# Optimization experiments

Hardware: AMD Instinct MI355X
Metric: run time of the kernel (lower is better)

The kernel has to match this reference:

```python
import jax, jax.numpy as jnp
import numpy as np

NUM_HEADS = 16
D_MODEL = 1024
HEAD_DIM = D_MODEL // NUM_HEADS
B, S = 2, 2048


def setup_inputs() -> dict:
    key = jax.random.key(0)
    ks = jax.random.split(key, 11)
    scale = 1.0 / np.sqrt(D_MODEL)
    inp = {
        'query': jax.random.normal(ks[0], (B, S, D_MODEL), jnp.float32),
        'key': jax.random.normal(ks[1], (B, S, D_MODEL), jnp.float32),
        'value': jax.random.normal(ks[2], (B, S, D_MODEL), jnp.float32),
        'Wq': jax.random.normal(ks[3], (D_MODEL, D_MODEL), jnp.float32) * scale,
        'bq': jnp.zeros((D_MODEL,), jnp.float32),
        'Wk': jax.random.normal(ks[4], (D_MODEL, D_MODEL), jnp.float32) * scale,
        'bk': jnp.zeros((D_MODEL,), jnp.float32),
        'Wv': jax.random.normal(ks[5], (D_MODEL, D_MODEL), jnp.float32) * scale,
        'bv': jnp.zeros((D_MODEL,), jnp.float32),
        'Wo': jax.random.normal(ks[6], (D_MODEL, D_MODEL), jnp.float32) * scale,
        'bo': jnp.zeros((D_MODEL,), jnp.float32),
    }
    return inp


def reference(query, key, value, Wq, bq, Wk, bk, Wv, bv, Wo, bo):
    b, s, _ = query.shape
    # Linear projections (torch Linear: x @ W.T + b; here W stored as [in,out])
    Q = query @ Wq + bq
    K = key @ Wk + bk
    V = value @ Wv + bv
    # [B, H, S, Dh]
    Q = Q.reshape(b, s, NUM_HEADS, HEAD_DIM).transpose(0, 2, 1, 3)
    K = K.reshape(b, -1, NUM_HEADS, HEAD_DIM).transpose(0, 2, 1, 3)
    V = V.reshape(b, -1, NUM_HEADS, HEAD_DIM).transpose(0, 2, 1, 3)
    scores = jnp.einsum('bhqd,bhkd->bhqk', Q, K) / jnp.sqrt(jnp.float32(HEAD_DIM)).astype(Q.dtype)
    attn = jax.nn.softmax(scores, axis=-1)
    ctx = jnp.einsum('bhqk,bhkd->bhqd', attn, V)
    ctx = ctx.transpose(0, 2, 1, 3).reshape(b, s, D_MODEL)
    return ctx @ Wo + bo
```

## Files before the change

### kernel.cpp

```cpp
#include <hip/hip_runtime.h>
#include <hip/hip_bf16.h>
#include <math.h>

#define NUM_HEADS 16
#define D_MODEL 1024
#define HEAD_DIM 64
#define BATCH 2
#define SEQ 2048
#define M_TOTAL (BATCH*SEQ)

typedef __bf16 bf16;
typedef __bf16 bf16x2 __attribute__((ext_vector_type(2)));
typedef __bf16 bf16x4 __attribute__((ext_vector_type(4)));
typedef __bf16 bf16x8 __attribute__((ext_vector_type(8)));
typedef float  floatx4  __attribute__((ext_vector_type(4)));
typedef float  floatx16 __attribute__((ext_vector_type(16)));
typedef unsigned int uintx2 __attribute__((ext_vector_type(2)));
typedef unsigned int uintx4 __attribute__((ext_vector_type(4)));

#define CLSCALE 0.180336884f

#if __has_builtin(__builtin_amdgcn_exp2f)
#define EXP2(x) __builtin_amdgcn_exp2f(x)
#else
#define EXP2(x) exp2f(x)
#endif

__device__ __forceinline__ void async_copy16(const bf16* g, bf16* l) {
    __builtin_amdgcn_global_load_lds(
        (const __attribute__((address_space(1))) void*)g,
        (__attribute__((address_space(3))) void*)l, 16, 0, 0);
}

__device__ __forceinline__ unsigned pk2(float lo, float hi) {
    bf16x2 t; t[0] = (bf16)lo; t[1] = (bf16)hi;
    return __builtin_bit_cast(unsigned, t);
}

__global__ __launch_bounds__(256)
void convert_kernel(const float* __restrict__ Wq, const float* __restrict__ Wk,
                    const float* __restrict__ Wv, const float* __restrict__ Wo,
                    const float* __restrict__ q, const float* __restrict__ k,
                    const float* __restrict__ v,
                    bf16* __restrict__ Wt, bf16* __restrict__ Xb)
{
    const int blk = blockIdx.x;
    const int tid = threadIdx.x;
    if (blk < 256) {
        const int wi  = blk >> 6;
        const int sub = blk & 63;
        const int xb  = sub & 3;
        const int yb  = sub >> 2;
        const float* W = (wi == 0) ? Wq : (wi == 1) ? Wk : (wi == 2) ? Wv : Wo;
        bf16* dstM = Wt + (size_t)wi * D_MODEL * D_MODEL;
        const int n  = xb * 256 + tid;
        const int k0 = yb * 64;
        bf16* dst = dstM + (size_t)n * D_MODEL + k0;
        #pragma unroll
        for (int jc = 0; jc < 8; ++jc) {
            bf16x8 w;
            #pragma unroll
            for (int j = 0; j < 8; ++j)
                w[j] = (bf16)W[(size_t)(k0 + jc * 8 + j) * D_MODEL + n];
            *(bf16x8*)(dst + jc * 8) = w;
        }
    } else {
        const int rem   = blk - 256;
        const int plane = rem >> 11;
        const int xb    = rem & 2047;
        const float* X = (plane == 0) ? q : (plane == 1) ? k : v;
        bf16* dst = Xb + (size_t)plane * M_TOTAL * D_MODEL;
        size_t i = ((size_t)xb * 256 + tid) * 8;
        const float4 u = *(const float4*)(X + i);
        const float4 w = *(const float4*)(X + i + 4);
        bf16x8 o;
        o[0] = (bf16)u.x; o[1] = (bf16)u.y; o[2] = (bf16)u.z; o[3] = (bf16)u.w;
        o[4] = (bf16)w.x; o[5] = (bf16)w.y; o[6] = (bf16)w.z; o[7] = (bf16)w.w;
        *(bf16x8*)(dst + i) = o;
    }
}

__global__ __launch_bounds__(256)
void proj_kernel(const bf16* __restrict__ Xb, const bf16* __restrict__ Wt,
                 const float* __restrict__ bq, const float* __restrict__ bk,
                 const float* __restrict__ bv,
                 bf16* __restrict__ Qo, bf16* __restrict__ Ko, bf16* __restrict__ Vto)
{
    const int lin  = blockIdx.x;
    const int xcd  = lin & 7;
    const int idx  = lin >> 3;
    const int nt   = idx & 7;
    const int t2   = idx >> 3;
    const int mloc = t2 & 3;
    const int which= t2 >> 2;
    const int tileM = (xcd * 4 + mloc) * 128;
    const int tileN = nt * 128;

    const bf16* X     = Xb + (size_t)which * M_TOTAL * D_MODEL;
    const bf16* Wm    = Wt + (size_t)which * D_MODEL * D_MODEL;
    const float* bias = (which == 0) ? bq : (which == 1) ? bk : bv;

    const int tid  = threadIdx.x;
    const int lane = tid & 63;
    const int wave = tid >> 6;
    const int quad = lane >> 4;
    const int l16  = lane & 15;

    __shared__ bf16 sA[2][4096];
    __shared__ bf16 sB[2][4096];

    floatx4 acc[4][4];
    const floatx4 z4 = {0.0f, 0.0f, 0.0f, 0.0f};
    #pragma unroll
    for (int i = 0; i < 4; i++)
        #pragma unroll
        for (int j = 0; j < 4; j++) acc[i][j] = z4;

    const int rC = ((tid >> 6) & 3) * 16 + (tid & 15);
    const int cC = ((tid >> 4) & 3) * 8;
    const bf16* gA0 = X  + (size_t)(tileM + rC) * D_MODEL + cC;
    const bf16* gA1 = gA0 + (size_t)64 * D_MODEL;
    const bf16* gB0 = Wm + (size_t)(tileN + rC) * D_MODEL + cC;
    const bf16* gB1 = gB0 + (size_t)64 * D_MODEL;

    async_copy16(gA0, &sA[0][tid * 8]);
    async_copy16(gA1, &sA[0][(tid + 256) * 8]);
    async_copy16(gB0, &sB[0][tid * 8]);
    async_copy16(gB1, &sB[0][(tid + 256) * 8]);

    const int fA = (wave >> 1) * 4;
    const int fB = (wave & 1) * 4;

    for (int kt = 0; kt < 32; ++kt) {
        const int p = kt & 1;
        __syncthreads();

        bf16x8 af[4], bfr[4];
        #pragma unroll
        for (int i = 0; i < 4; i++) af[i]  = *(const bf16x8*)&sA[p][((fA + i) * 64 + lane) * 8];
        #pragma unroll
        for (int j = 0; j < 4; j++) bfr[j] = *(const bf16x8*)&sB[p][((fB + j) * 64 + lane) * 8];

        if (kt < 31) {
            const int k0 = (kt + 1) * 32;
            async_copy16(gA0 + k0, &sA[p ^ 1][tid * 8]);
            async_copy16(gA1 + k0, &sA[p ^ 1][(tid + 256) * 8]);
            async_copy16(gB0 + k0, &sB[p ^ 1][tid * 8]);
            async_copy16(gB1 + k0, &sB[p ^ 1][(tid + 256) * 8]);
        }

        if (which != 2) {
            #pragma unroll
            for (int i = 0; i < 4; i++)
                #pragma unroll
                for (int j = 0; j < 4; j++)
                    acc[i][j] = __builtin_amdgcn_mfma_f32_16x16x32_bf16(af[i], bfr[j], acc[i][j], 0, 0, 0);
        } else {
            #pragma unroll
            for (int i = 0; i < 4; i++)
                #pragma unroll
                for (int j = 0; j < 4; j++)
                    acc[i][j] = __builtin_amdgcn_mfma_f32_16x16x32_bf16(bfr[i], af[j], acc[i][j], 0, 0, 0);
        }
    }

    const int wm = (wave >> 1) * 64;
    const int wn = (wave & 1) * 64;

    if (which != 2) {
        bf16* out = (which == 0) ? Qo : Ko;
        const float oscale = (which == 0) ? CLSCALE : 1.0f;
        #pragma unroll
        for (int i = 0; i < 4; i++) {
            int mbase = tileM + wm + i * 16 + quad * 4;
            #pragma unroll
            for (int j = 0; j < 4; j++) {
                int n = tileN + wn + j * 16 + l16;
                float bb = bias[n];
                int h = n >> 6, d = n & 63;
                #pragma unroll
                for (int r = 0; r < 4; r++) {
                    int mm = mbase + r;
                    int b = mm >> 11, s = mm & 2047;
                    out[(((size_t)(b * NUM_HEADS + h)) * SEQ + s) * HEAD_DIM + d] =
                        (bf16)((acc[i][j][r] + bb) * oscale);
                }
            }
        }
    } else {
        #pragma unroll
        for (int i = 0; i < 4; i++) {
            #pragma unroll
            for (int r = 0; r < 4; r++) {
                int n = tileN + wn + i * 16 + quad * 4 + r;
                float bb = bias[n];
                int h = n >> 6, d = n & 63;
                #pragma unroll
                for (int j = 0; j < 4; j++) {
                    int m = tileM + wm + j * 16 + l16;
                    int b = m >> 11, s = m & 2047;
                    Vto[(((size_t)(b * NUM_HEADS + h)) * HEAD_DIM + d) * SEQ + s] =
                        (bf16)(acc[i][j][r] + bb);
                }
            }
        }
    }
}

__global__ __launch_bounds__(256)
void attn_kernel(const bf16* __restrict__ Q, const bf16* __restrict__ K,
                 const bf16* __restrict__ Vt, bf16* __restrict__ Ctx)
{
    const int lin    = blockIdx.x;
    const int xcd    = lin & 7;
    const int rest   = lin >> 3;
    const int superg = rest >> 5;
    const int qi     = rest & 31;
    const int bh     = superg * 8 + xcd;
    const int b      = bh >> 4, h = bh & 15;
    const int q0     = qi * 64;

    const int tid  = threadIdx.x;
    const int lane = tid & 63;
    const int wave = tid >> 6;
    const int half = lane >> 5;
    const int m31  = lane & 31;
    const int xs   = m31 & 7;

    const int qsub  = wave & 1;
    const int kjsub = wave >> 1;

    __shared__ bf16 sK[2][64 * 64];
    __shared__ bf16 sV[2][64 * 64];
    __shared__ float sL[64];

    const bf16* Qb  = Q  + ((size_t)bh * SEQ + q0) * HEAD_DIM;
    const bf16* Kb  = K  + (size_t)bh * SEQ * HEAD_DIM;
    const bf16* Vtb = Vt + (size_t)bh * HEAD_DIM * SEQ;

    bf16x8 bQ[4];
    #pragma unroll
    for (int s = 0; s < 4; s++)
        bQ[s] = *(const bf16x8*)(Qb + (size_t)(qsub * 32 + m31) * HEAD_DIM + s * 16 + half * 8);

    #pragma unroll
    for (int it = 0; it < 2; ++it) {
        int c    = tid + it * 256;
        int row  = c >> 3;
        int scol = ((c & 7) ^ (row & 7)) * 8;
        async_copy16(Kb  + (size_t)row * HEAD_DIM + scol, &sK[0][c * 8]);
        async_copy16(Vtb + (size_t)row * SEQ + scol,      &sV[0][c * 8]);
    }

    floatx16 o0, o1;
    #pragma unroll
    for (int r = 0; r < 16; r++) { o0[r] = 0.0f; o1[r] = 0.0f; }
    float lp = 0.0f;

    for (int kt = 0; kt < SEQ / 64; ++kt) {
        const int p = kt & 1;
        __syncthreads();

        bf16x8 aK[4];
        #pragma unroll
        for (int s = 0; s < 4; s++)
            aK[s] = *(const bf16x8*)&sK[p][(kjsub * 32 + m31) * 64 + (((2 * s + half) ^ xs) * 8)];

        if (kt + 1 < SEQ / 64) {
            #pragma unroll
            for (int it = 0; it < 2; ++it) {
                int c    = tid + it * 256;
                int row  = c >> 3;
                int scol = ((c & 7) ^ (row & 7)) * 8;
                async_copy16(Kb  + (size_t)((kt + 1) * 64 + row) * HEAD_DIM + scol,
                             &sK[p ^ 1][c * 8]);
                async_copy16(Vtb + (size_t)row * SEQ + (kt + 1) * 64 + scol,
                             &sV[p ^ 1][c * 8]);
            }
        }

        floatx16 sc;
        #pragma unroll
        for (int r = 0; r < 16; r++) sc[r] = 0.0f;
        __builtin_amdgcn_s_setprio(1);
        #pragma unroll
        for (int s = 0; s < 4; s++)
            sc = __builtin_amdgcn_mfma_f32_32x32x16_bf16(aK[s], bQ[s], sc, 0, 0, 0);
        __builtin_amdgcn_s_setprio(0);

        #pragma unroll
        for (int r = 0; r < 16; r++) sc[r] = EXP2(sc[r]);
        float ls = 0.0f;
        #pragma unroll
        for (int r = 0; r < 16; r++) ls += sc[r];
        lp += ls;

        bf16x8 bP[2];
        #pragma unroll
        for (int s = 0; s < 2; s++) {
            const int bs = 8 * s;
            unsigned x = pk2(sc[bs + 0], sc[bs + 1]);
            unsigned z = pk2(sc[bs + 2], sc[bs + 3]);
            unsigned y = pk2(sc[bs + 4], sc[bs + 5]);
            unsigned w = pk2(sc[bs + 6], sc[bs + 7]);
            auto r0 = __builtin_amdgcn_permlane32_swap(x, y, false, false);
            auto r1 = __builtin_amdgcn_permlane32_swap(z, w, false, false);
            uintx4 bp;
            bp[0] = r0[0]; bp[1] = r1[0]; bp[2] = r0[1]; bp[3] = r1[1];
            bP[s] = __builtin_bit_cast(bf16x8, bp);
        }

        __builtin_amdgcn_s_setprio(1);
        #pragma unroll
        for (int s = 0; s < 2; s++) {
            int ch = ((4 * kjsub + 2 * s + half) ^ xs) * 8;
            bf16x8 a0 = *(const bf16x8*)&sV[p][(size_t)m31 * 64 + ch];
            bf16x8 a1 = *(const bf16x8*)&sV[p][(size_t)(32 + m31) * 64 + ch];
            o0 = __builtin_amdgcn_mfma_f32_32x32x16_bf16(a0, bP[s], o0, 0, 0, 0);
            o1 = __builtin_amdgcn_mfma_f32_32x32x16_bf16(a1, bP[s], o1, 0, 0, 0);
        }
        __builtin_amdgcn_s_setprio(0);
    }

    lp += __shfl_xor(lp, 32, 64);

    __syncthreads();
    float* fO = (qsub == 0) ? (float*)&sK[0][0] : (float*)&sK[1][0];
    if (kjsub == 1) {
        #pragma unroll
        for (int r = 0; r < 16; r++) {
            fO[r * 64 + lane]        = o0[r];
            fO[1024 + r * 64 + lane] = o1[r];
        }
        if (half == 0) sL[qsub * 32 + m31] = lp;
    }
    __syncthreads();
    if (kjsub == 0) {
        #pragma unroll
        for (int r = 0; r < 16; r++) {
            o0[r] += fO[r * 64 + lane];
            o1[r] += fO[1024 + r * 64 + lane];
        }
        float denom = lp + sL[qsub * 32 + m31];
        float inv = 1.0f / denom;

        int q = q0 + qsub * 32 + m31;
        size_t base = ((size_t)b * SEQ + q) * D_MODEL + h * HEAD_DIM;
        #pragma unroll
        for (int rg = 0; rg < 4; rg++) {
            int d0 = rg * 8 + half * 4;
            bf16x4 w0, w1;
            #pragma unroll
            for (int i = 0; i < 4; i++) {
                w0[i] = (bf16)(o0[rg * 4 + i] * inv);
                w1[i] = (bf16)(o1[rg * 4 + i] * inv);
            }
            *(bf16x4*)&Ctx[base + d0]      = w0;
            *(bf16x4*)&Ctx[base + 32 + d0] = w1;
        }
    }
}

__global__ __launch_bounds__(256)
void out_proj_kernel(const bf16* __restrict__ A, const bf16* __restrict__ Wto,
                     const float* __restrict__ bias, float* __restrict__ Out)
{
    const int lin  = blockIdx.x;
    const int xcd  = lin & 7;
    const int idx  = lin >> 3;
    const int nt   = idx & 7;
    const int mloc = idx >> 3;
    const int tileM = (xcd * 8 + mloc) * 64;
    const int tileN = nt * 128;

    const int tid  = threadIdx.x;
    const int lane = tid & 63;
    const int wave = tid >> 6;
    const int quad = lane >> 4;
    const int l16  = lane & 15;

    __shared__ bf16 sA[2][2048];
    __shared__ bf16 sB[2][4096];

    floatx4 acc[2][4];
    const floatx4 z4 = {0.0f, 0.0f, 0.0f, 0.0f};
    #pragma unroll
    for (int i = 0; i < 2; i++)
        #pragma unroll
        for (int j = 0; j < 4; j++) acc[i][j] = z4;

    const int rA = ((tid >> 7) & 1) * 32 + ((tid >> 6) & 1) * 16 + (tid & 15);
    const int rB = ((tid >> 6) & 3) * 16 + (tid & 15);
    const int cC = ((tid >> 4) & 3) * 8;
    const bf16* gA0 = A   + (size_t)(tileM + rA) * D_MODEL + cC;
    const bf16* gB0 = Wto + (size_t)(tileN + rB) * D_MODEL + cC;
    const bf16* gB1 = gB0 + (size_t)64 * D_MODEL;

    async_copy16(gA0, &sA[0][tid * 8]);
    async_copy16(gB0, &sB[0][tid * 8]);
    async_copy16(gB1, &sB[0][(tid + 256) * 8]);

    const int fA = (wave >> 1) * 2;
    const int fB = (wave & 1) * 4;

    for (int kt = 0; kt < 32; ++kt) {
        const int p = kt & 1;
        __syncthreads();

        bf16x8 af[2], bfr[4];
        #pragma unroll
        for (int i = 0; i < 2; i++) af[i]  = *(const bf16x8*)&sA[p][((fA + i) * 64 + lane) * 8];
        #pragma unroll
        for (int j = 0; j < 4; j++) bfr[j] = *(const bf16x8*)&sB[p][((fB + j) * 64 + lane) * 8];

        if (kt < 31) {
            const int k0 = (kt + 1) * 32;
            async_copy16(gA0 + k0, &sA[p ^ 1][tid * 8]);
            async_copy16(gB0 + k0, &sB[p ^ 1][tid * 8]);
            async_copy16(gB1 + k0, &sB[p ^ 1][(tid + 256) * 8]);
        }

        #pragma unroll
        for (int i = 0; i < 2; i++)
            #pragma unroll
            for (int j = 0; j < 4; j++)
                acc[i][j] = __builtin_amdgcn_mfma_f32_16x16x32_bf16(af[i], bfr[j], acc[i][j], 0, 0, 0);
    }

    const int wm = (wave >> 1) * 32;
    const int wn = (wave & 1) * 64;

    #pragma unroll
    for (int i = 0; i < 2; i++) {
        int mbase = tileM + wm + i * 16 + quad * 4;
        #pragma unroll
        for (int j = 0; j < 4; j++) {
            int n = tileN + wn + j * 16 + l16;
            float bb = bias[n];
            #pragma unroll
            for (int r = 0; r < 4; r++)
                Out[(size_t)(mbase + r) * D_MODEL + n] = acc[i][j][r] + bb;
        }
    }
}

extern "C" void kernel_launch(void* const* d_in, const int* in_sizes, int n_in,
                              void* d_out, int out_size, void* d_ws, size_t ws_size,
                              hipStream_t stream)
{
    const float* q  = (const float*)d_in[0];
    const float* k  = (const float*)d_in[1];
    const float* v  = (const float*)d_in[2];
    const float* Wq = (const float*)d_in[3];
    const float* bq = (const float*)d_in[4];
    const float* Wk = (const float*)d_in[5];
    const float* bk = (const float*)d_in[6];
    const float* Wv = (const float*)d_in[7];
    const float* bv = (const float*)d_in[8];
    const float* Wo = (const float*)d_in[9];
    const float* bo = (const float*)d_in[10];
    float* out = (float*)d_out;

    const size_t PLANE = (size_t)M_TOTAL * D_MODEL;
    bf16* Qb = (bf16*)d_ws;
    bf16* Kb = Qb + PLANE;
    bf16* Vt = Kb + PLANE;
    bf16* Cb = Vt + PLANE;
    bf16* Wt = Cb + PLANE;
    bf16* Xb = Wt + 4 * (size_t)D_MODEL * D_MODEL;

    convert_kernel<<<dim3(6400), 256, 0, stream>>>(Wq, Wk, Wv, Wo, q, k, v, Wt, Xb);
    proj_kernel<<<dim3(768), 256, 0, stream>>>(Xb, Wt, bq, bk, bv, Qb, Kb, Vt);
    attn_kernel<<<dim3(1024), 256, 0, stream>>>(Qb, Kb, Vt, Cb);
    out_proj_kernel<<<dim3(512), 256, 0, stream>>>(Cb, Wt + 3 * (size_t)D_MODEL * D_MODEL, bo, out);
}
```

Measured before the change: 254.4 us.

## Triple-buffer QKV and output projection GEMM loads with partial vmcnt waits

Both projection GEMM kernels now use three shared-memory stages and prefetch two k-tiles ahead. The full __syncthreads is replaced by an explicit s_waitcnt vmcnt(N) plus s_barrier, so only the oldest stage has to land before compute. The aim is to hide global-to-LDS copy latency behind the MFMA work. In exchange it uses 1.5x the LDS, which may lower occupancy, and it relies on the vmcnt counts matching the number of async copies issued per stage.

```diff
diff --git a/kernel.cpp b/kernel.cpp
--- a/kernel.cpp
+++ b/kernel.cpp
@@ -106,8 +106,8 @@
     const int quad = lane >> 4;
     const int l16  = lane & 15;
 
-    __shared__ bf16 sA[2][4096];
-    __shared__ bf16 sB[2][4096];
+    __shared__ bf16 sA[3][4096];
+    __shared__ bf16 sB[3][4096];
 
     floatx4 acc[4][4];
     const floatx4 z4 = {0.0f, 0.0f, 0.0f, 0.0f};
@@ -123,17 +123,25 @@
     const bf16* gB0 = Wm + (size_t)(tileN + rC) * D_MODEL + cC;
     const bf16* gB1 = gB0 + (size_t)64 * D_MODEL;
 
-    async_copy16(gA0, &sA[0][tid * 8]);
-    async_copy16(gA1, &sA[0][(tid + 256) * 8]);
-    async_copy16(gB0, &sB[0][tid * 8]);
-    async_copy16(gB1, &sB[0][(tid + 256) * 8]);
+    auto stage = [&](int buf, int k0) {
+        async_copy16(gA0 + k0, &sA[buf][tid * 8]);
+        async_copy16(gA1 + k0, &sA[buf][(tid + 256) * 8]);
+        async_copy16(gB0 + k0, &sB[buf][tid * 8]);
+        async_copy16(gB1 + k0, &sB[buf][(tid + 256) * 8]);
+    };
+
+    stage(0, 0);
+    stage(1, 32);
 
     const int fA = (wave >> 1) * 4;
     const int fB = (wave & 1) * 4;
 
+    int p = 0;
     for (int kt = 0; kt < 32; ++kt) {
-        const int p = kt & 1;
-        __syncthreads();
+        if (kt < 31) asm volatile("s_waitcnt vmcnt(4)" ::: "memory");
+        else         asm volatile("s_waitcnt vmcnt(0)" ::: "memory");
+        __builtin_amdgcn_s_barrier();
+        __builtin_amdgcn_sched_barrier(0);
 
         bf16x8 af[4], bfr[4];
         #pragma unroll
@@ -141,12 +149,9 @@
         #pragma unroll
         for (int j = 0; j < 4; j++) bfr[j] = *(const bf16x8*)&sB[p][((fB + j) * 64 + lane) * 8];
 
-        if (kt < 31) {
-            const int k0 = (kt + 1) * 32;
-            async_copy16(gA0 + k0, &sA[p ^ 1][tid * 8]);
-            async_copy16(gA1 + k0, &sA[p ^ 1][(tid + 256) * 8]);
-            async_copy16(gB0 + k0, &sB[p ^ 1][tid * 8]);
-            async_copy16(gB1 + k0, &sB[p ^ 1][(tid + 256) * 8]);
+        if (kt + 2 < 32) {
+            int pw = p + 2; if (pw >= 3) pw -= 3;
+            stage(pw, (kt + 2) * 32);
         }
 
         if (which != 2) {
@@ -162,6 +167,7 @@
                 for (int j = 0; j < 4; j++)
                     acc[i][j] = __builtin_amdgcn_mfma_f32_16x16x32_bf16(bfr[i], af[j], acc[i][j], 0, 0, 0);
         }
+        p = (p == 2) ? 0 : p + 1;
     }
 
     const int wm = (wave >> 1) * 64;
@@ -379,8 +385,8 @@
     const int quad = lane >> 4;
     const int l16  = lane & 15;
 
-    __shared__ bf16 sA[2][2048];
-    __shared__ bf16 sB[2][4096];
+    __shared__ bf16 sA[3][2048];
+    __shared__ bf16 sB[3][4096];
 
     floatx4 acc[2][4];
     const floatx4 z4 = {0.0f, 0.0f, 0.0f, 0.0f};
@@ -396,16 +402,24 @@
     const bf16* gB0 = Wto + (size_t)(tileN + rB) * D_MODEL + cC;
     const bf16* gB1 = gB0 + (size_t)64 * D_MODEL;
 
-    async_copy16(gA0, &sA[0][tid * 8]);
-    async_copy16(gB0, &sB[0][tid * 8]);
-    async_copy16(gB1, &sB[0][(tid + 256) * 8]);
+    auto stage = [&](int buf, int k0) {
+        async_copy16(gA0 + k0, &sA[buf][tid * 8]);
+        async_copy16(gB0 + k0, &sB[buf][tid * 8]);
+        async_copy16(gB1 + k0, &sB[buf][(tid + 256) * 8]);
+    };
+
+    stage(0, 0);
+    stage(1, 32);
 
     const int fA = (wave >> 1) * 2;
     const int fB = (wave & 1) * 4;
 
+    int p = 0;
     for (int kt = 0; kt < 32; ++kt) {
-        const int p = kt & 1;
-        __syncthreads();
+        if (kt < 31) asm volatile("s_waitcnt vmcnt(3)" ::: "memory");
+        else         asm volatile("s_waitcnt vmcnt(0)" ::: "memory");
+        __builtin_amdgcn_s_barrier();
+        __builtin_amdgcn_sched_barrier(0);
 
         bf16x8 af[2], bfr[4];
         #pragma unroll
@@ -413,11 +427,9 @@
         #pragma unroll
         for (int j = 0; j < 4; j++) bfr[j] = *(const bf16x8*)&sB[p][((fB + j) * 64 + lane) * 8];
 
-        if (kt < 31) {
-            const int k0 = (kt + 1) * 32;
-            async_copy16(gA0 + k0, &sA[p ^ 1][tid * 8]);
-            async_copy16(gB0 + k0, &sB[p ^ 1][tid * 8]);
-            async_copy16(gB1 + k0, &sB[p ^ 1][(tid + 256) * 8]);
+        if (kt + 2 < 32) {
+            int pw = p + 2; if (pw >= 3) pw -= 3;
+            stage(pw, (kt + 2) * 32);
         }
 
         #pragma unroll
@@ -425,6 +437,7 @@
             #pragma unroll
             for (int j = 0; j < 4; j++)
                 acc[i][j] = __builtin_amdgcn_mfma_f32_16x16x32_bf16(af[i], bfr[j], acc[i][j], 0, 0, 0);
+        p = (p == 2) ? 0 : p + 1;
     }
 
     const int wm = (wave >> 1) * 32;
```

New measurement: 252.3 us. Within noise of the previous version (-0.8%).

## Fuse fp32-to-bf16 activation conversion into projection GEMM and single-buffer GEMM tiles

Applied to the files above, without the earlier changes.

The separate pass that converts the query, key and value activations to bf16 is removed. The projection GEMM now loads fp32 activations directly, converts them in registers and stores bf16 into shared memory, which avoids writing and re-reading a full bf16 copy of the inputs. Both the projection and output-projection GEMMs also drop double-buffered shared-memory prefetch in favour of a single buffer with two barriers per k-step. That frees LDS but exposes global-load latency that the prefetch used to hide.

```diff
diff --git a/kernel.cpp b/kernel.cpp
--- a/kernel.cpp
+++ b/kernel.cpp
@@ -15,7 +15,6 @@
 typedef __bf16 bf16x8 __attribute__((ext_vector_type(8)));
 typedef float  floatx4  __attribute__((ext_vector_type(4)));
 typedef float  floatx16 __attribute__((ext_vector_type(16)));
-typedef unsigned int uintx2 __attribute__((ext_vector_type(2)));
 typedef unsigned int uintx4 __attribute__((ext_vector_type(4)));
 
 #define CLSCALE 0.180336884f
@@ -40,48 +39,32 @@
 __global__ __launch_bounds__(256)
 void convert_kernel(const float* __restrict__ Wq, const float* __restrict__ Wk,
                     const float* __restrict__ Wv, const float* __restrict__ Wo,
-                    const float* __restrict__ q, const float* __restrict__ k,
-                    const float* __restrict__ v,
-                    bf16* __restrict__ Wt, bf16* __restrict__ Xb)
+                    bf16* __restrict__ Wt)
 {
     const int blk = blockIdx.x;
     const int tid = threadIdx.x;
-    if (blk < 256) {
-        const int wi  = blk >> 6;
-        const int sub = blk & 63;
-        const int xb  = sub & 3;
-        const int yb  = sub >> 2;
-        const float* W = (wi == 0) ? Wq : (wi == 1) ? Wk : (wi == 2) ? Wv : Wo;
-        bf16* dstM = Wt + (size_t)wi * D_MODEL * D_MODEL;
-        const int n  = xb * 256 + tid;
-        const int k0 = yb * 64;
-        bf16* dst = dstM + (size_t)n * D_MODEL + k0;
-        #pragma unroll
-        for (int jc = 0; jc < 8; ++jc) {
-            bf16x8 w;
-            #pragma unroll
-            for (int j = 0; j < 8; ++j)
-                w[j] = (bf16)W[(size_t)(k0 + jc * 8 + j) * D_MODEL + n];
-            *(bf16x8*)(dst + jc * 8) = w;
-        }
-    } else {
-        const int rem   = blk - 256;
-        const int plane = rem >> 11;
-        const int xb    = rem & 2047;
-        const float* X = (plane == 0) ? q : (plane == 1) ? k : v;
-        bf16* dst = Xb + (size_t)plane * M_TOTAL * D_MODEL;
-        size_t i = ((size_t)xb * 256 + tid) * 8;
-        const float4 u = *(const float4*)(X + i);
-        const float4 w = *(const float4*)(X + i + 4);
-        bf16x8 o;
-        o[0] = (bf16)u.x; o[1] = (bf16)u.y; o[2] = (bf16)u.z; o[3] = (bf16)u.w;
-        o[4] = (bf16)w.x; o[5] = (bf16)w.y; o[6] = (bf16)w.z; o[7] = (bf16)w.w;
-        *(bf16x8*)(dst + i) = o;
+    const int wi  = blk >> 6;
+    const int sub = blk & 63;
+    const int xb  = sub & 3;
+    const int yb  = sub >> 2;
+    const float* W = (wi == 0) ? Wq : (wi == 1) ? Wk : (wi == 2) ? Wv : Wo;
+    bf16* dstM = Wt + (size_t)wi * D_MODEL * D_MODEL;
+    const int n  = xb * 256 + tid;
+    const int k0 = yb * 64;
+    bf16* dst = dstM + (size_t)n * D_MODEL + k0;
+    #pragma unroll
+    for (int jc = 0; jc < 8; ++jc) {
+        bf16x8 w;
+        #pragma unroll
+        for (int j = 0; j < 8; ++j)
+            w[j] = (bf16)W[(size_t)(k0 + jc * 8 + j) * D_MODEL + n];
+        *(bf16x8*)(dst + jc * 8) = w;
     }
 }
 
 __global__ __launch_bounds__(256)
-void proj_kernel(const bf16* __restrict__ Xb, const bf16* __restrict__ Wt,
+void proj_kernel(const float* __restrict__ Xq, const float* __restrict__ Xk,
+                 const float* __restrict__ Xv, const bf16* __restrict__ Wt,
                  const float* __restrict__ bq, const float* __restrict__ bk,
                  const float* __restrict__ bv,
                  bf16* __restrict__ Qo, bf16* __restrict__ Ko, bf16* __restrict__ Vto)
@@ -96,7 +79,7 @@
     const int tileM = (xcd * 4 + mloc) * 128;
     const int tileN = nt * 128;
 
-    const bf16* X     = Xb + (size_t)which * M_TOTAL * D_MODEL;
+    const float* X32  = (which == 0) ? Xq : (which == 1) ? Xk : Xv;
     const bf16* Wm    = Wt + (size_t)which * D_MODEL * D_MODEL;
     const float* bias = (which == 0) ? bq : (which == 1) ? bk : bv;
 
@@ -106,8 +89,8 @@
     const int quad = lane >> 4;
     const int l16  = lane & 15;
 
-    __shared__ bf16 sA[2][4096];
-    __shared__ bf16 sB[2][4096];
+    __shared__ bf16 sA[4096];
+    __shared__ bf16 sB[4096];
 
     floatx4 acc[4][4];
     const floatx4 z4 = {0.0f, 0.0f, 0.0f, 0.0f};
@@ -118,36 +101,40 @@
 
     const int rC = ((tid >> 6) & 3) * 16 + (tid & 15);
     const int cC = ((tid >> 4) & 3) * 8;
-    const bf16* gA0 = X  + (size_t)(tileM + rC) * D_MODEL + cC;
-    const bf16* gA1 = gA0 + (size_t)64 * D_MODEL;
-    const bf16* gB0 = Wm + (size_t)(tileN + rC) * D_MODEL + cC;
-    const bf16* gB1 = gB0 + (size_t)64 * D_MODEL;
-
-    async_copy16(gA0, &sA[0][tid * 8]);
-    async_copy16(gA1, &sA[0][(tid + 256) * 8]);
-    async_copy16(gB0, &sB[0][tid * 8]);
-    async_copy16(gB1, &sB[0][(tid + 256) * 8]);
+    const float* gA0 = X32 + (size_t)(tileM + rC) * D_MODEL + cC;
+    const float* gA1 = gA0 + (size_t)64 * D_MODEL;
+    const bf16*  gB0 = Wm  + (size_t)(tileN + rC) * D_MODEL + cC;
+    const bf16*  gB1 = gB0 + (size_t)64 * D_MODEL;
 
     const int fA = (wave >> 1) * 4;
     const int fB = (wave & 1) * 4;
 
     for (int kt = 0; kt < 32; ++kt) {
-        const int p = kt & 1;
+        const int k0 = kt * 32;
         __syncthreads();
 
+        async_copy16(gB0 + k0, &sB[tid * 8]);
+        async_copy16(gB1 + k0, &sB[(tid + 256) * 8]);
+
+        float4 u0 = *(const float4*)(gA0 + k0);
+        float4 v0 = *(const float4*)(gA0 + k0 + 4);
+        float4 u1 = *(const float4*)(gA1 + k0);
+        float4 v1 = *(const float4*)(gA1 + k0 + 4);
+        bf16x8 a0, a1;
+        a0[0] = (bf16)u0.x; a0[1] = (bf16)u0.y; a0[2] = (bf16)u0.z; a0[3] = (bf16)u0.w;
+        a0[4] = (bf16)v0.x; a0[5] = (bf16)v0.y; a0[6] = (bf16)v0.z; a0[7] = (bf16)v0.w;
+        a1[0] = (bf16)u1.x; a1[1] = (bf16)u1.y; a1[2] = (bf16)u1.z; a1[3] = (bf16)u1.w;
+        a1[4] = (bf16)v1.x; a1[5] = (bf16)v1.y; a1[6] = (bf16)v1.z; a1[7] = (bf16)v1.w;
+        *(bf16x8*)&sA[tid * 8]         = a0;
+        *(bf16x8*)&sA[(tid + 256) * 8] = a1;
+
+        __syncthreads();
+
         bf16x8 af[4], bfr[4];
         #pragma unroll
-        for (int i = 0; i < 4; i++) af[i]  = *(const bf16x8*)&sA[p][((fA + i) * 64 + lane) * 8];
-        #pragma unroll
-        for (int j = 0; j < 4; j++) bfr[j] = *(const bf16x8*)&sB[p][((fB + j) * 64 + lane) * 8];
-
-        if (kt < 31) {
-            const int k0 = (kt + 1) * 32;
-            async_copy16(gA0 + k0, &sA[p ^ 1][tid * 8]);
-            async_copy16(gA1 + k0, &sA[p ^ 1][(tid + 256) * 8]);
-            async_copy16(gB0 + k0, &sB[p ^ 1][tid * 8]);
-            async_copy16(gB1 + k0, &sB[p ^ 1][(tid + 256) * 8]);
-        }
+        for (int i = 0; i < 4; i++) af[i]  = *(const bf16x8*)&sA[((fA + i) * 64 + lane) * 8];
+        #pragma unroll
+        for (int j = 0; j < 4; j++) bfr[j] = *(const bf16x8*)&sB[((fB + j) * 64 + lane) * 8];
 
         if (which != 2) {
             #pragma unroll
@@ -379,8 +366,8 @@
     const int quad = lane >> 4;
     const int l16  = lane & 15;
 
-    __shared__ bf16 sA[2][2048];
-    __shared__ bf16 sB[2][4096];
+    __shared__ bf16 sA[2048];
+    __shared__ bf16 sB[4096];
 
     floatx4 acc[2][4];
     const floatx4 z4 = {0.0f, 0.0f, 0.0f, 0.0f};
@@ -389,36 +376,30 @@
         #pragma unroll
         for (int j = 0; j < 4; j++) acc[i][j] = z4;
 
-    const int rA = ((tid >> 7) & 1) * 32 + ((tid >> 6) & 1) * 16 + (tid & 15);
-    const int rB = ((tid >> 6) & 3) * 16 + (tid & 15);
+    const int rC = ((tid >> 6) & 3) * 16 + (tid & 15);
     const int cC = ((tid >> 4) & 3) * 8;
-    const bf16* gA0 = A   + (size_t)(tileM + rA) * D_MODEL + cC;
-    const bf16* gB0 = Wto + (size_t)(tileN + rB) * D_MODEL + cC;
+    const bf16* gA0 = A   + (size_t)(tileM + rC) * D_MODEL + cC;
+    const bf16* gB0 = Wto + (size_t)(tileN + rC) * D_MODEL + cC;
     const bf16* gB1 = gB0 + (size_t)64 * D_MODEL;
-
-    async_copy16(gA0, &sA[0][tid * 8]);
-    async_copy16(gB0, &sB[0][tid * 8]);
-    async_copy16(gB1, &sB[0][(tid + 256) * 8]);
 
     const int fA = (wave >> 1) * 2;
     const int fB = (wave & 1) * 4;
 
     for (int kt = 0; kt < 32; ++kt) {
-        const int p = kt & 1;
+        const int k0 = kt * 32;
         __syncthreads();
 
+        async_copy16(gA0 + k0, &sA[tid * 8]);
+        async_copy16(gB0 + k0, &sB[tid * 8]);
+        async_copy16(gB1 + k0, &sB[(tid + 256) * 8]);
+
+        __syncthreads();
+
         bf16x8 af[2], bfr[4];
         #pragma unroll
-        for (int i = 0; i < 2; i++) af[i]  = *(const bf16x8*)&sA[p][((fA + i) * 64 + lane) * 8];
-        #pragma unroll
-        for (int j = 0; j < 4; j++) bfr[j] = *(const bf16x8*)&sB[p][((fB + j) * 64 + lane) * 8];
-
-        if (kt < 31) {
-            const int k0 = (kt + 1) * 32;
-            async_copy16(gA0 + k0, &sA[p ^ 1][tid * 8]);
-            async_copy16(gB0 + k0, &sB[p ^ 1][tid * 8]);
-            async_copy16(gB1 + k0, &sB[p ^ 1][(tid + 256) * 8]);
-        }
+        for (int i = 0; i < 2; i++) af[i]  = *(const bf16x8*)&sA[((fA + i) * 64 + lane) * 8];
+        #pragma unroll
+        for (int j = 0; j < 4; j++) bfr[j] = *(const bf16x8*)&sB[((fB + j) * 64 + lane) * 8];
 
         #pragma unroll
         for (int i = 0; i < 2; i++)
@@ -467,10 +448,9 @@
     bf16* Vt = Kb + PLANE;
     bf16* Cb = Vt + PLANE;
     bf16* Wt = Cb + PLANE;
-    bf16* Xb = Wt + 4 * (size_t)D_MODEL * D_MODEL;
-
-    convert_kernel<<<dim3(6400), 256, 0, stream>>>(Wq, Wk, Wv, Wo, q, k, v, Wt, Xb);
-    proj_kernel<<<dim3(768), 256, 0, stream>>>(Xb, Wt, bq, bk, bv, Qb, Kb, Vt);
+
+    convert_kernel<<<dim3(256), 256, 0, stream>>>(Wq, Wk, Wv, Wo, Wt);
+    proj_kernel<<<dim3(768), 256, 0, stream>>>(q, k, v, Wt, bq, bk, bv, Qb, Kb, Vt);
     attn_kernel<<<dim3(1024), 256, 0, stream>>>(Qb, Kb, Vt, Cb);
     out_proj_kernel<<<dim3(512), 256, 0, stream>>>(Cb, Wt + 3 * (size_t)D_MODEL * D_MODEL, bo, out);
 }
```

Result: slower. 291.8 us (+14.7%).

## Shrink projection GEMM tiles and drop double buffering for more blocks

Applied to the files above, without the earlier changes.

The QKV projection tile goes from 128x128 to 64x128 and the output projection tile from 64x128 to 64x64, doubling the grid sizes of both kernels. The LDS double buffer with prefetch is replaced by a single buffer, loaded and then synchronised before compute on every k step. The intent is more blocks and occupancy with less LDS per block. In exchange, global loads no longer overlap with MFMA work, there are two barriers per iteration, and operand reuse per block is lower.

```diff
diff --git a/kernel.cpp b/kernel.cpp
--- a/kernel.cpp
+++ b/kernel.cpp
@@ -15,7 +15,6 @@
 typedef __bf16 bf16x8 __attribute__((ext_vector_type(8)));
 typedef float  floatx4  __attribute__((ext_vector_type(4)));
 typedef float  floatx16 __attribute__((ext_vector_type(16)));
-typedef unsigned int uintx2 __attribute__((ext_vector_type(2)));
 typedef unsigned int uintx4 __attribute__((ext_vector_type(4)));
 
 #define CLSCALE 0.180336884f
@@ -91,9 +90,9 @@
     const int idx  = lin >> 3;
     const int nt   = idx & 7;
     const int t2   = idx >> 3;
-    const int mloc = t2 & 3;
-    const int which= t2 >> 2;
-    const int tileM = (xcd * 4 + mloc) * 128;
+    const int mloc = t2 & 7;
+    const int which= t2 >> 3;
+    const int tileM = (xcd * 8 + mloc) * 64;
     const int tileN = nt * 128;
 
     const bf16* X     = Xb + (size_t)which * M_TOTAL * D_MODEL;
@@ -106,72 +105,64 @@
     const int quad = lane >> 4;
     const int l16  = lane & 15;
 
-    __shared__ bf16 sA[2][4096];
-    __shared__ bf16 sB[2][4096];
-
-    floatx4 acc[4][4];
+    __shared__ bf16 sA[4 * 64 * 8];
+    __shared__ bf16 sB[8 * 64 * 8];
+
+    floatx4 acc[2][4];
     const floatx4 z4 = {0.0f, 0.0f, 0.0f, 0.0f};
     #pragma unroll
-    for (int i = 0; i < 4; i++)
+    for (int i = 0; i < 2; i++)
         #pragma unroll
         for (int j = 0; j < 4; j++) acc[i][j] = z4;
 
     const int rC = ((tid >> 6) & 3) * 16 + (tid & 15);
     const int cC = ((tid >> 4) & 3) * 8;
-    const bf16* gA0 = X  + (size_t)(tileM + rC) * D_MODEL + cC;
-    const bf16* gA1 = gA0 + (size_t)64 * D_MODEL;
+    const bf16* gA  = X  + (size_t)(tileM + rC) * D_MODEL + cC;
     const bf16* gB0 = Wm + (size_t)(tileN + rC) * D_MODEL + cC;
     const bf16* gB1 = gB0 + (size_t)64 * D_MODEL;
 
-    async_copy16(gA0, &sA[0][tid * 8]);
-    async_copy16(gA1, &sA[0][(tid + 256) * 8]);
-    async_copy16(gB0, &sB[0][tid * 8]);
-    async_copy16(gB1, &sB[0][(tid + 256) * 8]);
-
-    const int fA = (wave >> 1) * 4;
+    const int fA = (wave >> 1) * 2;
     const int fB = (wave & 1) * 4;
 
     for (int kt = 0; kt < 32; ++kt) {
-        const int p = kt & 1;
+        const int k0 = kt * 32;
         __syncthreads();
 
-        bf16x8 af[4], bfr[4];
-        #pragma unroll
-        for (int i = 0; i < 4; i++) af[i]  = *(const bf16x8*)&sA[p][((fA + i) * 64 + lane) * 8];
-        #pragma unroll
-        for (int j = 0; j < 4; j++) bfr[j] = *(const bf16x8*)&sB[p][((fB + j) * 64 + lane) * 8];
-
-        if (kt < 31) {
-            const int k0 = (kt + 1) * 32;
-            async_copy16(gA0 + k0, &sA[p ^ 1][tid * 8]);
-            async_copy16(gA1 + k0, &sA[p ^ 1][(tid + 256) * 8]);
-            async_copy16(gB0 + k0, &sB[p ^ 1][tid * 8]);
-            async_copy16(gB1 + k0, &sB[p ^ 1][(tid + 256) * 8]);
-        }
+        async_copy16(gA  + k0, &sA[tid * 8]);
+        async_copy16(gB0 + k0, &sB[tid * 8]);
+        async_copy16(gB1 + k0, &sB[(tid + 256) * 8]);
+
+        __syncthreads();
+
+        bf16x8 af[2], bfr[4];
+        #pragma unroll
+        for (int i = 0; i < 2; i++) af[i]  = *(const bf16x8*)&sA[((fA + i) * 64 + lane) * 8];
+        #pragma unroll
+        for (int j = 0; j < 4; j++) bfr[j] = *(const bf16x8*)&sB[((fB + j) * 64 + lane) * 8];
 
         if (which != 2) {
             #pragma unroll
-            for (int i = 0; i < 4; i++)
+            for (int i = 0; i < 2; i++)
                 #pragma unroll
                 for (int j = 0; j < 4; j++)
                     acc[i][j] = __builtin_amdgcn_mfma_f32_16x16x32_bf16(af[i], bfr[j], acc[i][j], 0, 0, 0);
         } else {
             #pragma unroll
-            for (int i = 0; i < 4; i++)
+            for (int i = 0; i < 2; i++)
                 #pragma unroll
                 for (int j = 0; j < 4; j++)
-                    acc[i][j] = __builtin_amdgcn_mfma_f32_16x16x32_bf16(bfr[i], af[j], acc[i][j], 0, 0, 0);
-        }
-    }
-
-    const int wm = (wave >> 1) * 64;
+                    acc[i][j] = __builtin_amdgcn_mfma_f32_16x16x32_bf16(bfr[j], af[i], acc[i][j], 0, 0, 0);
+        }
+    }
+
+    const int wm = (wave >> 1) * 32;
     const int wn = (wave & 1) * 64;
 
     if (which != 2) {
         bf16* out = (which == 0) ? Qo : Ko;
         const float oscale = (which == 0) ? CLSCALE : 1.0f;
         #pragma unroll
-        for (int i = 0; i < 4; i++) {
+        for (int i = 0; i < 2; i++) {
             int mbase = tileM + wm + i * 16 + quad * 4;
             #pragma unroll
             for (int j = 0; j < 4; j++) {
@@ -189,15 +180,15 @@
         }
     } else {
         #pragma unroll
-        for (int i = 0; i < 4; i++) {
+        for (int j = 0; j < 4; j++) {
             #pragma unroll
             for (int r = 0; r < 4; r++) {
-                int n = tileN + wn + i * 16 + quad * 4 + r;
+                int n = tileN + wn + j * 16 + quad * 4 + r;
                 float bb = bias[n];
                 int h = n >> 6, d = n & 63;
                 #pragma unroll
-                for (int j = 0; j < 4; j++) {
-                    int m = tileM + wm + j * 16 + l16;
+                for (int i = 0; i < 2; i++) {
+                    int m = tileM + wm + i * 16 + l16;
                     int b = m >> 11, s = m & 2047;
                     Vto[(((size_t)(b * NUM_HEADS + h)) * HEAD_DIM + d) * SEQ + s] =
                         (bf16)(acc[i][j][r] + bb);
@@ -368,10 +359,10 @@
     const int lin  = blockIdx.x;
     const int xcd  = lin & 7;
     const int idx  = lin >> 3;
-    const int nt   = idx & 7;
-    const int mloc = idx >> 3;
+    const int nt   = idx & 15;
+    const int mloc = idx >> 4;
     const int tileM = (xcd * 8 + mloc) * 64;
-    const int tileN = nt * 128;
+    const int tileN = nt * 64;
 
     const int tid  = threadIdx.x;
     const int lane = tid & 63;
@@ -379,62 +370,54 @@
     const int quad = lane >> 4;
     const int l16  = lane & 15;
 
-    __shared__ bf16 sA[2][2048];
-    __shared__ bf16 sB[2][4096];
-
-    floatx4 acc[2][4];
+    __shared__ bf16 sA[4 * 64 * 8];
+    __shared__ bf16 sB[4 * 64 * 8];
+
+    floatx4 acc[2][2];
     const floatx4 z4 = {0.0f, 0.0f, 0.0f, 0.0f};
     #pragma unroll
     for (int i = 0; i < 2; i++)
         #pragma unroll
-        for (int j = 0; j < 4; j++) acc[i][j] = z4;
-
-    const int rA = ((tid >> 7) & 1) * 32 + ((tid >> 6) & 1) * 16 + (tid & 15);
-    const int rB = ((tid >> 6) & 3) * 16 + (tid & 15);
+        for (int j = 0; j < 2; j++) acc[i][j] = z4;
+
+    const int rC = ((tid >> 6) & 3) * 16 + (tid & 15);
     const int cC = ((tid >> 4) & 3) * 8;
-    const bf16* gA0 = A   + (size_t)(tileM + rA) * D_MODEL + cC;
-    const bf16* gB0 = Wto + (size_t)(tileN + rB) * D_MODEL + cC;
-    const bf16* gB1 = gB0 + (size_t)64 * D_MODEL;
-
-    async_copy16(gA0, &sA[0][tid * 8]);
-    async_copy16(gB0, &sB[0][tid * 8]);
-    async_copy16(gB1, &sB[0][(tid + 256) * 8]);
+    const bf16* gA = A   + (size_t)(tileM + rC) * D_MODEL + cC;
+    const bf16* gB = Wto + (size_t)(tileN + rC) * D_MODEL + cC;
 
     const int fA = (wave >> 1) * 2;
-    const int fB = (wave & 1) * 4;
+    const int fB = (wave & 1) * 2;
 
     for (int kt = 0; kt < 32; ++kt) {
-        const int p = kt & 1;
+        const int k0 = kt * 32;
         __syncthreads();
 
-        bf16x8 af[2], bfr[4];
-        #pragma unroll
-        for (int i = 0; i < 2; i++) af[i]  = *(const bf16x8*)&sA[p][((fA + i) * 64 + lane) * 8];
-        #pragma unroll
-        for (int j = 0; j < 4; j++) bfr[j] = *(const bf16x8*)&sB[p][((fB + j) * 64 + lane) * 8];
-
-        if (kt < 31) {
-            const int k0 = (kt + 1) * 32;
-            async_copy16(gA0 + k0, &sA[p ^ 1][tid * 8]);
-            async_copy16(gB0 + k0, &sB[p ^ 1][tid * 8]);
-            async_copy16(gB1 + k0, &sB[p ^ 1][(tid + 256) * 8]);
-        }
+        async_copy16(gA + k0, &sA[tid * 8]);
+        async_copy16(gB + k0, &sB[tid * 8]);
+
+        __syncthreads();
+
+        bf16x8 af[2], bfr[2];
+        #pragma unroll
+        for (int i = 0; i < 2; i++) af[i]  = *(const bf16x8*)&sA[((fA + i) * 64 + lane) * 8];
+        #pragma unroll
+        for (int j = 0; j < 2; j++) bfr[j] = *(const bf16x8*)&sB[((fB + j) * 64 + lane) * 8];
 
         #pragma unroll
         for (int i = 0; i < 2; i++)
             #pragma unroll
-            for (int j = 0; j < 4; j++)
+            for (int j = 0; j < 2; j++)
                 acc[i][j] = __builtin_amdgcn_mfma_f32_16x16x32_bf16(af[i], bfr[j], acc[i][j], 0, 0, 0);
     }
 
     const int wm = (wave >> 1) * 32;
-    const int wn = (wave & 1) * 64;
+    const int wn = (wave & 1) * 32;
 
     #pragma unroll
     for (int i = 0; i < 2; i++) {
         int mbase = tileM + wm + i * 16 + quad * 4;
         #pragma unroll
-        for (int j = 0; j < 4; j++) {
+        for (int j = 0; j < 2; j++) {
             int n = tileN + wn + j * 16 + l16;
             float bb = bias[n];
             #pragma unroll
@@ -470,7 +453,7 @@
     bf16* Xb = Wt + 4 * (size_t)D_MODEL * D_MODEL;
 
     convert_kernel<<<dim3(6400), 256, 0, stream>>>(Wq, Wk, Wv, Wo, q, k, v, Wt, Xb);
-    proj_kernel<<<dim3(768), 256, 0, stream>>>(Xb, Wt, bq, bk, bv, Qb, Kb, Vt);
+    proj_kernel<<<dim3(1536), 256, 0, stream>>>(Xb, Wt, bq, bk, bv, Qb, Kb, Vt);
     attn_kernel<<<dim3(1024), 256, 0, stream>>>(Qb, Kb, Vt, Cb);
-    out_proj_kernel<<<dim3(512), 256, 0, stream>>>(Cb, Wt + 3 * (size_t)D_MODEL * D_MODEL, bo, out);
-}
+    out_proj_kernel<<<dim3(1024), 256, 0, stream>>>(Cb, Wt + 3 * (size_t)D_MODEL * D_MODEL, bo, out);
+}
```

After: 278.1 us. +9.3%, slower.
